# Kernel tuning notes

Measured on AMD Instinct MI355X. Metric: run time of the kernel, lower is better.

The kernel has to match this reference:

```python
import jax, jax.numpy as jnp
import numpy as np

B, SEQ, C, H, OVERLAP, G, K, D = 16, 8192, 192, 16, 4, 6, 1024, 8
FIX = H * C                      # 3072 (proj_ratio = 1.0, no in/out proj)
DG = (FIX * OVERLAP) // G        # 2048, per-group dim
W = SEQ // H                     # 512 time frames
T = W // OVERLAP                 # 128 grouped frames


def _l2norm(x, eps=1e-12):
    return x / jnp.clip(jnp.linalg.norm(x, axis=-1, keepdims=True), eps)


def setup_inputs() -> dict:
    key = jax.random.key(0)
    k0, k1, k2, k3 = jax.random.split(key, 4)
    z = jax.random.normal(k0, (B, SEQ, C), jnp.float32)
    # stacked per-group parameters (all groups have equal dim DG)
    proj_down = jax.random.normal(k1, (G, DG, D), jnp.float32) * (DG ** -0.5)
    proj_up = jax.random.normal(k2, (G, D, DG), jnp.float32) * (D ** -0.5)
    codebooks = jax.random.normal(k3, (G, K, D), jnp.float32)
    return {"z": z, "proj_down": proj_down, "proj_up": proj_up, "codebooks": codebooks}


def reference(z, proj_down, proj_up, codebooks):
    # --- pre_process: 'b (h w) c -> b w (c h)' then fold overlap ---
    zz = z.reshape(B, H, W, C)                      # b h w c
    zz = jnp.transpose(zz, (0, 2, 3, 1))            # b w c h
    zz = zz.reshape(B, W, FIX)                      # b w (c h)
    zz = zz.reshape(B, T, OVERLAP * FIX)            # fold overlap frames
    zg = zz.reshape(B, T, G, DG)                    # split into G groups

    # --- per-group codebook VQ (vectorized over G) ---
    z_e = jnp.einsum('btgd,gde->btge', zg, proj_down)           # (B,T,G,D)
    sim = jnp.einsum('btge,gke->btgk', _l2norm(z_e), _l2norm(codebooks))
    code = jnp.argmax(sim, axis=-1)                             # (B,T,G)
    gidx = jnp.arange(G)[None, None, :]
    z_q = codebooks[gidx, code]                                 # (B,T,G,D)

    # per-batch-element losses, mean over (T, D) per group, averaged over groups
    commitment = jnp.mean((z_e - jax.lax.stop_gradient(z_q)) ** 2, axis=(1, 3)).mean(axis=1)
    codebook_l = jnp.mean((jax.lax.stop_gradient(z_e) - z_q) ** 2, axis=(1, 3)).mean(axis=1)

    # straight-through estimator + up projection
    z_q_st = z_e + jax.lax.stop_gradient(z_q - z_e)
    z_up = jnp.einsum('btge,ged->btgd', z_q_st, proj_up)        # (B,T,G,DG)
    z_up = z_up.reshape(B, T, OVERLAP * FIX)

    # --- post_process: unfold overlap, 'b w (c h) -> b (h w) c' ---
    out = z_up.reshape(B, W, FIX)                   # b w (c h)
    out = out.reshape(B, W, C, H)
    out = jnp.transpose(out, (0, 3, 1, 2))          # b h w c
    out = out.reshape(B, SEQ, C)
    return out, commitment, codebook_l
```

## Files before the change

kernel.cpp:

```cpp
#include <hip/hip_runtime.h>
#include <math.h>

#define B_ 16
#define SEQ_ 8192
#define C_ 192
#define H_ 16
#define OV_ 4
#define G_ 6
#define K_ 1024
#define D_ 8
#define DG_ 2048
#define W_ 512
#define T_ 128
#define TT 4
#define OUT_ELEMS (B_ * SEQ_ * C_)



__global__ __launch_bounds__(256) void vq_prep(
    const float* __restrict__ pd, const float* __restrict__ pu,
    const float* __restrict__ cb,
    float* __restrict__ pd_p, float* __restrict__ pu_p,
    double* __restrict__ cbn, float* __restrict__ loss_slots)
{
  int i = blockIdx.x * 256 + threadIdx.x;
  if (i < 98304) {
    int e = i & 7, dp = (i >> 3) & 2047, g = i >> 14;
    int h = dp >> 7, ul = dp & 127, d = (ul << 4) + h;
    pd_p[i] = pd[(g << 14) + (d << 3) + e];
  } else if (i < 196608) {
    int i2 = i - 98304;
    int dp = i2 & 2047, e = (i2 >> 11) & 7, g = i2 >> 14;
    int h = dp >> 7, ul = dp & 127, d = (ul << 4) + h;
    pu_p[i2] = pu[(g << 14) + (e << 11) + d];
  } else if (i < 202752) {
    int j = i - 196608;
    const float* row = cb + (j << 3);
    double ss = 0.0;
    #pragma unroll
    for (int e = 0; e < 8; ++e) { double x = (double)row[e]; ss += x * x; }
    double inv = 1.0 / fmax(sqrt(ss), 1e-12);
    #pragma unroll
    for (int e = 0; e < 8; ++e) cbn[(j << 3) + e] = (double)row[e] * inv;
  } else if (i < 202784) {
    loss_slots[i - 202752] = 0.0f;
  }
}

__global__ __launch_bounds__(256) void vq_main(
    const float* __restrict__ z, const float* __restrict__ cb,
    const float* __restrict__ pd_p, const float* __restrict__ pu_p,
    const double* __restrict__ cbn,
    float* __restrict__ out, float* __restrict__ loss_slots)
{
  __shared__ __align__(16) float zs[TT * DG_];
  __shared__ double ze_d[TT * 8];
  __shared__ float  zq_s[TT * 8];
  __shared__ double wr_s[4][TT];
  __shared__ int    wr_k[4][TT];
  __shared__ float  lossv[TT];

  const int tid = threadIdx.x;
  const int tc  = blockIdx.x;
  const int g   = blockIdx.y;
  const int b   = blockIdx.z;

  const float* zb = z + (size_t)b * (SEQ_ * C_);

  #pragma unroll
  for (int t = 0; t < TT; ++t) {
    int wbase = (tc * TT + t) * OV_;
    #pragma unroll
    for (int j = 0; j < 2; ++j) {
      int v  = j * 256 + tid;
      int h  = v >> 5;
      int ul = (v & 31) << 2;
      int u  = (g << 7) + ul;
      int o  = (u * 683) >> 17;
      int c  = u - o * 192;
      const float4 val = *(const float4*)(zb + (h * 512 + wbase + o) * 192 + c);
      *(float4*)(&zs[t * DG_ + (h << 7) + ul]) = val;
    }
  }
  __syncthreads();

  double acc[TT][8];
  #pragma unroll
  for (int t = 0; t < TT; ++t)
    #pragma unroll
    for (int e = 0; e < 8; ++e) acc[t][e] = 0.0;

  #pragma unroll
  for (int i = 0; i < 8; ++i) {
    int dp = i * 256 + tid;
    const float4 p0 = *(const float4*)(pd_p + ((((g << 11) + dp) << 3)));
    const float4 p1 = *(const float4*)(pd_p + ((((g << 11) + dp) << 3) + 4));
    #pragma unroll
    for (int t = 0; t < TT; ++t) {
      double zv = (double)zs[t * DG_ + dp];
      acc[t][0] = fma(zv, (double)p0.x, acc[t][0]);
      acc[t][1] = fma(zv, (double)p0.y, acc[t][1]);
      acc[t][2] = fma(zv, (double)p0.z, acc[t][2]);
      acc[t][3] = fma(zv, (double)p0.w, acc[t][3]);
      acc[t][4] = fma(zv, (double)p1.x, acc[t][4]);
      acc[t][5] = fma(zv, (double)p1.y, acc[t][5]);
      acc[t][6] = fma(zv, (double)p1.z, acc[t][6]);
      acc[t][7] = fma(zv, (double)p1.w, acc[t][7]);
    }
  }

  double* part_d = (double*)zs;
  #pragma unroll
  for (int r = 0; r < 2; ++r) {
    __syncthreads();
    #pragma unroll
    for (int kkl = 0; kkl < 16; ++kkl) {
      int kk = r * 16 + kkl;
      part_d[kkl * 256 + tid] = acc[kk >> 3][kk & 7];
    }
    __syncthreads();
    int kkl = tid >> 4, jj = tid & 15;
    double partial = 0.0;
    #pragma unroll
    for (int s = 0; s < 16; ++s) {
      int p = (s + tid) & 15;
      partial += part_d[kkl * 256 + jj * 16 + p];
    }
    partial += __shfl_down(partial, 8);
    partial += __shfl_down(partial, 4);
    partial += __shfl_down(partial, 2);
    partial += __shfl_down(partial, 1);
    if (jj == 0) ze_d[r * 16 + kkl] = partial;
  }
  __syncthreads();

  double cd[4][8];
  #pragma unroll
  for (int q = 0; q < 4; ++q) {
    const double* cr = cbn + (((g << 10) + (q << 8) + tid) << 3);
    #pragma unroll
    for (int e = 0; e < 8; ++e) cd[q][e] = cr[e];
  }
  double bs[TT]; int bk[TT];
  #pragma unroll
  for (int t = 0; t < TT; ++t) {
    double zr[8];
    #pragma unroll
    for (int e = 0; e < 8; ++e) zr[e] = ze_d[t * 8 + e];
    bs[t] = -1.0e300; bk[t] = 0x7fffffff;
    #pragma unroll
    for (int q = 0; q < 4; ++q) {
      double s = 0.0;
      #pragma unroll
      for (int e = 0; e < 8; ++e) s = fma(zr[e], cd[q][e], s);
      int k = (q << 8) + tid;
      if (s > bs[t]) { bs[t] = s; bk[t] = k; }
    }
  }
  #pragma unroll
  for (int m = 32; m >= 1; m >>= 1) {
    #pragma unroll
    for (int t = 0; t < TT; ++t) {
      double os = __shfl_xor(bs[t], m);
      int    ok = __shfl_xor(bk[t], m);
      if (os > bs[t] || (os == bs[t] && ok < bk[t])) { bs[t] = os; bk[t] = ok; }
    }
  }
  int wv = tid >> 6;
  if ((tid & 63) == 0) {
    #pragma unroll
    for (int t = 0; t < TT; ++t) { wr_s[wv][t] = bs[t]; wr_k[wv][t] = bk[t]; }
  }
  __syncthreads();
  if (tid < TT) {
    int t = tid;
    double s0 = wr_s[0][t]; int k0 = wr_k[0][t];
    #pragma unroll
    for (int w2 = 1; w2 < 4; ++w2) {
      double s1 = wr_s[w2][t]; int k1 = wr_k[w2][t];
      if (s1 > s0 || (s1 == s0 && k1 < k0)) { s0 = s1; k0 = k1; }
    }
    const float* crow = cb + (((g << 10) + k0) << 3);
    double l = 0.0;
    #pragma unroll
    for (int e = 0; e < 8; ++e) {
      float qv = crow[e];
      zq_s[t * 8 + e] = qv;
      double dd = ze_d[t * 8 + e] - (double)qv;
      l = fma(dd, dd, l);
    }
    lossv[t] = (float)l;
  }
  __syncthreads();
  if (tid == 0) {
    float l = (lossv[0] + lossv[1] + lossv[2] + lossv[3]) * (1.0f / (T_ * D_ * G_));
    atomicAdd(loss_slots + b, l);
    atomicAdd(loss_slots + 16 + b, l);
  }

  float zqr[TT][8];
  #pragma unroll
  for (int t = 0; t < TT; ++t)
    #pragma unroll
    for (int e = 0; e < 8; ++e) zqr[t][e] = zq_s[t * 8 + e];

  #pragma unroll
  for (int j = 0; j < 8; ++j) {
    int dp = j * 256 + tid;
    int h = dp >> 7, ul = dp & 127;
    int u = (g << 7) + ul;
    int o = (u * 683) >> 17;
    int c = u - o * 192;
    float pv[8];
    #pragma unroll
    for (int e = 0; e < 8; ++e) pv[e] = pu_p[(g << 14) + (e << 11) + dp];
    size_t base = ((size_t)(b * SEQ_) + h * 512 + tc * (TT * OV_) + o) * 192 + c;
    #pragma unroll
    for (int t = 0; t < TT; ++t) {
      float v = 0.f;
      #pragma unroll
      for (int e = 0; e < 8; ++e) v = fmaf(zqr[t][e], pv[e], v);
      out[base + (size_t)(t * OV_ * 192)] = v;
    }
  }
}

extern "C" void kernel_launch(void* const* d_in, const int* in_sizes, int n_in,
                              void* d_out, int out_size, void* d_ws, size_t ws_size,
                              hipStream_t stream)
{
  const float* z  = (const float*)d_in[0];
  const float* pd = (const float*)d_in[1];
  const float* pu = (const float*)d_in[2];
  const float* cb = (const float*)d_in[3];
  float* out = (float*)d_out;
  float* loss_slots = out + OUT_ELEMS;

  float*  pd_p = (float*)d_ws;
  float*  pu_p = pd_p + 98304;
  double* cbn  = (double*)(pu_p + 98304);

  vq_prep<<<793, 256, 0, stream>>>(pd, pu, cb, pd_p, pu_p, cbn, loss_slots);
  dim3 grid(T_ / TT, G_, B_);
  vq_main<<<grid, 256, 0, stream>>>(z, cb, pd_p, pu_p, cbn, out, loss_slots);
}
```

Measured before the change: 212.8 us.

## Stream z directly from global, vectorize output stores, halve frames per block

Removes the shared-memory staging of z: each thread loads float4 chunks of z and the matching projection rows and accumulates in double directly. TT drops from 4 to 2, doubling the grid and shrinking register and LDS use, and the reduction is reworked for the smaller tile. The up-projection now writes float4 stores instead of scalar strided stores. The trade-off is that pd_p, pu_p and the codebook are reloaded by twice as many blocks.

```diff
diff --git a/kernel.cpp b/kernel.cpp
--- a/kernel.cpp
+++ b/kernel.cpp
@@ -12,9 +12,8 @@
 #define DG_ 2048
 #define W_ 512
 #define T_ 128
-#define TT 4
+#define TT 2
 #define OUT_ELEMS (B_ * SEQ_ * C_)
-
 
 
 __global__ __launch_bounds__(256) void vq_prep(
@@ -53,7 +52,7 @@
     const double* __restrict__ cbn,
     float* __restrict__ out, float* __restrict__ loss_slots)
 {
-  __shared__ __align__(16) float zs[TT * DG_];
+  __shared__ __align__(16) double red[8 * 256];
   __shared__ double ze_d[TT * 8];
   __shared__ float  zq_s[TT * 8];
   __shared__ double wr_s[4][TT];
@@ -67,93 +66,89 @@
 
   const float* zb = z + (size_t)b * (SEQ_ * C_);
 
-  #pragma unroll
-  for (int t = 0; t < TT; ++t) {
-    int wbase = (tc * TT + t) * OV_;
-    #pragma unroll
-    for (int j = 0; j < 2; ++j) {
-      int v  = j * 256 + tid;
-      int h  = v >> 5;
-      int ul = (v & 31) << 2;
-      int u  = (g << 7) + ul;
-      int o  = (u * 683) >> 17;
-      int c  = u - o * 192;
-      const float4 val = *(const float4*)(zb + (h * 512 + wbase + o) * 192 + c);
-      *(float4*)(&zs[t * DG_ + (h << 7) + ul]) = val;
-    }
+  double acc[TT][8];
+  #pragma unroll
+  for (int t = 0; t < TT; ++t)
+    #pragma unroll
+    for (int e = 0; e < 8; ++e) acc[t][e] = 0.0;
+
+  #pragma unroll
+  for (int j = 0; j < 2; ++j) {
+    int v   = j * 256 + tid;
+    int h   = v >> 5;
+    int ul4 = (v & 31) << 2;
+    int u   = (g << 7) + ul4;
+    int o   = (u * 683) >> 17;
+    int c   = u - o * 192;
+    int dp  = (h << 7) + ul4;
+    const float4* pdp = (const float4*)(pd_p + (((size_t)(g << 11) + dp) << 3));
+    float4 p[8];
+    #pragma unroll
+    for (int r = 0; r < 8; ++r) p[r] = pdp[r];
+    #pragma unroll
+    for (int t = 0; t < TT; ++t) {
+      int w = ((tc * TT + t) << 2) + o;
+      float4 zv = *(const float4*)(zb + (size_t)(h * 512 + w) * 192 + c);
+      float zc[4] = {zv.x, zv.y, zv.z, zv.w};
+      #pragma unroll
+      for (int r = 0; r < 4; ++r) {
+        double zd = (double)zc[r];
+        acc[t][0] = fma(zd, (double)p[2*r].x,   acc[t][0]);
+        acc[t][1] = fma(zd, (double)p[2*r].y,   acc[t][1]);
+        acc[t][2] = fma(zd, (double)p[2*r].z,   acc[t][2]);
+        acc[t][3] = fma(zd, (double)p[2*r].w,   acc[t][3]);
+        acc[t][4] = fma(zd, (double)p[2*r+1].x, acc[t][4]);
+        acc[t][5] = fma(zd, (double)p[2*r+1].y, acc[t][5]);
+        acc[t][6] = fma(zd, (double)p[2*r+1].z, acc[t][6]);
+        acc[t][7] = fma(zd, (double)p[2*r+1].w, acc[t][7]);
+      }
+    }
+  }
+
+  #pragma unroll
+  for (int r2 = 0; r2 < 2; ++r2) {
+    if (r2) __syncthreads();
+    #pragma unroll
+    for (int kkl = 0; kkl < 8; ++kkl) {
+      int kk = r2 * 8 + kkl;
+      red[kkl * 256 + tid] = acc[kk >> 3][kk & 7];
+    }
+    __syncthreads();
+    int kkl = tid >> 5, jj = tid & 31;
+    double partial = 0.0;
+    #pragma unroll
+    for (int s = 0; s < 8; ++s)
+      partial += red[kkl * 256 + s * 32 + jj];
+    partial += __shfl_down(partial, 16, 32);
+    partial += __shfl_down(partial, 8, 32);
+    partial += __shfl_down(partial, 4, 32);
+    partial += __shfl_down(partial, 2, 32);
+    partial += __shfl_down(partial, 1, 32);
+    if (jj == 0) ze_d[r2 * 8 + kkl] = partial;
   }
   __syncthreads();
 
-  double acc[TT][8];
+  double zr[TT][8];
   #pragma unroll
   for (int t = 0; t < TT; ++t)
     #pragma unroll
-    for (int e = 0; e < 8; ++e) acc[t][e] = 0.0;
-
-  #pragma unroll
-  for (int i = 0; i < 8; ++i) {
-    int dp = i * 256 + tid;
-    const float4 p0 = *(const float4*)(pd_p + ((((g << 11) + dp) << 3)));
-    const float4 p1 = *(const float4*)(pd_p + ((((g << 11) + dp) << 3) + 4));
-    #pragma unroll
-    for (int t = 0; t < TT; ++t) {
-      double zv = (double)zs[t * DG_ + dp];
-      acc[t][0] = fma(zv, (double)p0.x, acc[t][0]);
-      acc[t][1] = fma(zv, (double)p0.y, acc[t][1]);
-      acc[t][2] = fma(zv, (double)p0.z, acc[t][2]);
-      acc[t][3] = fma(zv, (double)p0.w, acc[t][3]);
-      acc[t][4] = fma(zv, (double)p1.x, acc[t][4]);
-      acc[t][5] = fma(zv, (double)p1.y, acc[t][5]);
-      acc[t][6] = fma(zv, (double)p1.z, acc[t][6]);
-      acc[t][7] = fma(zv, (double)p1.w, acc[t][7]);
-    }
-  }
-
-  double* part_d = (double*)zs;
-  #pragma unroll
-  for (int r = 0; r < 2; ++r) {
-    __syncthreads();
-    #pragma unroll
-    for (int kkl = 0; kkl < 16; ++kkl) {
-      int kk = r * 16 + kkl;
-      part_d[kkl * 256 + tid] = acc[kk >> 3][kk & 7];
-    }
-    __syncthreads();
-    int kkl = tid >> 4, jj = tid & 15;
-    double partial = 0.0;
-    #pragma unroll
-    for (int s = 0; s < 16; ++s) {
-      int p = (s + tid) & 15;
-      partial += part_d[kkl * 256 + jj * 16 + p];
-    }
-    partial += __shfl_down(partial, 8);
-    partial += __shfl_down(partial, 4);
-    partial += __shfl_down(partial, 2);
-    partial += __shfl_down(partial, 1);
-    if (jj == 0) ze_d[r * 16 + kkl] = partial;
-  }
-  __syncthreads();
-
-  double cd[4][8];
+    for (int e = 0; e < 8; ++e) zr[t][e] = ze_d[t * 8 + e];
+
+  double bs[TT]; int bk[TT];
+  #pragma unroll
+  for (int t = 0; t < TT; ++t) { bs[t] = -1.0e300; bk[t] = 0x7fffffff; }
   #pragma unroll
   for (int q = 0; q < 4; ++q) {
-    const double* cr = cbn + (((g << 10) + (q << 8) + tid) << 3);
-    #pragma unroll
-    for (int e = 0; e < 8; ++e) cd[q][e] = cr[e];
-  }
-  double bs[TT]; int bk[TT];
-  #pragma unroll
-  for (int t = 0; t < TT; ++t) {
-    double zr[8];
-    #pragma unroll
-    for (int e = 0; e < 8; ++e) zr[e] = ze_d[t * 8 + e];
-    bs[t] = -1.0e300; bk[t] = 0x7fffffff;
-    #pragma unroll
-    for (int q = 0; q < 4; ++q) {
+    const double* cr = cbn + (((size_t)(g << 10) + (q << 8) + tid) << 3);
+    double cdv[8];
+    #pragma unroll
+    for (int e = 0; e < 8; ++e) cdv[e] = cr[e];
+    int k = (q << 8) + tid;
+    #pragma unroll
+    for (int t = 0; t < TT; ++t) {
       double s = 0.0;
       #pragma unroll
-      for (int e = 0; e < 8; ++e) s = fma(zr[e], cd[q][e], s);
-      int k = (q << 8) + tid;
+      for (int e = 0; e < 8; ++e) s = fma(zr[t][e], cdv[e], s);
       if (s > bs[t]) { bs[t] = s; bk[t] = k; }
     }
   }
@@ -180,7 +175,7 @@
       double s1 = wr_s[w2][t]; int k1 = wr_k[w2][t];
       if (s1 > s0 || (s1 == s0 && k1 < k0)) { s0 = s1; k0 = k1; }
     }
-    const float* crow = cb + (((g << 10) + k0) << 3);
+    const float* crow = cb + (((size_t)(g << 10) + k0) << 3);
     double l = 0.0;
     #pragma unroll
     for (int e = 0; e < 8; ++e) {
@@ -193,7 +188,7 @@
   }
   __syncthreads();
   if (tid == 0) {
-    float l = (lossv[0] + lossv[1] + lossv[2] + lossv[3]) * (1.0f / (T_ * D_ * G_));
+    float l = (lossv[0] + lossv[1]) * (1.0f / (T_ * D_ * G_));
     atomicAdd(loss_slots + b, l);
     atomicAdd(loss_slots + 16 + b, l);
   }
@@ -205,22 +200,32 @@
     for (int e = 0; e < 8; ++e) zqr[t][e] = zq_s[t * 8 + e];
 
   #pragma unroll
-  for (int j = 0; j < 8; ++j) {
-    int dp = j * 256 + tid;
-    int h = dp >> 7, ul = dp & 127;
-    int u = (g << 7) + ul;
-    int o = (u * 683) >> 17;
-    int c = u - o * 192;
-    float pv[8];
-    #pragma unroll
-    for (int e = 0; e < 8; ++e) pv[e] = pu_p[(g << 14) + (e << 11) + dp];
-    size_t base = ((size_t)(b * SEQ_) + h * 512 + tc * (TT * OV_) + o) * 192 + c;
-    #pragma unroll
-    for (int t = 0; t < TT; ++t) {
-      float v = 0.f;
+  for (int j = 0; j < 2; ++j) {
+    int v   = j * 256 + tid;
+    int h   = v >> 5;
+    int ul4 = (v & 31) << 2;
+    int u   = (g << 7) + ul4;
+    int o   = (u * 683) >> 17;
+    int c   = u - o * 192;
+    int dp  = (h << 7) + ul4;
+    float4 pu4[8];
+    #pragma unroll
+    for (int e = 0; e < 8; ++e)
+      pu4[e] = *(const float4*)(pu_p + (size_t)(g << 14) + (e << 11) + dp);
+    #pragma unroll
+    for (int t = 0; t < TT; ++t) {
+      float4 ov;
+      ov.x = 0.f; ov.y = 0.f; ov.z = 0.f; ov.w = 0.f;
       #pragma unroll
-      for (int e = 0; e < 8; ++e) v = fmaf(zqr[t][e], pv[e], v);
-      out[base + (size_t)(t * OV_ * 192)] = v;
+      for (int e = 0; e < 8; ++e) {
+        float zq = zqr[t][e];
+        ov.x = fmaf(zq, pu4[e].x, ov.x);
+        ov.y = fmaf(zq, pu4[e].y, ov.y);
+        ov.z = fmaf(zq, pu4[e].z, ov.z);
+        ov.w = fmaf(zq, pu4[e].w, ov.w);
+      }
+      int w = ((tc * TT + t) << 2) + o;
+      *(float4*)(out + ((size_t)(b * SEQ_) + h * 512 + w) * 192 + c) = ov;
     }
   }
 }
```

After: 274.1 us. 1.29x slower.
